# Kernel optimization log

Measured on AMD Instinct MI355X. Metric: run time of the kernel, lower is better.

## Reference

```python
import jax, jax.numpy as jnp
import numpy as np

B, L = 2048, 64          # sentence pairs, leaves per balanced binary tree
V, IN, M, HID, NC = 50000, 300, 150, 50, 5


def setup_inputs() -> dict:
    key = jax.random.key(0)
    ks = jax.random.split(key, 16)
    lin = lambda k, fi, fo: jax.random.normal(k, (fi, fo), jnp.float32) / np.sqrt(fi).astype(np.float32)
    bias = lambda k, fo: jax.random.normal(k, (fo,), jnp.float32) * 0.01
    return {
        "ltokens": jax.random.randint(ks[0], (B, L), 0, V, dtype=jnp.int32),
        "rtokens": jax.random.randint(ks[1], (B, L), 0, V, dtype=jnp.int32),
        "emb":   jax.random.normal(ks[2], (V, IN), jnp.float32),
        "Wioux": lin(ks[3], IN, 3 * M), "bioux": bias(ks[4], 3 * M),
        "Wiouh": lin(ks[5], M, 3 * M), "biouh": bias(ks[6], 3 * M),
        "Wfx":   lin(ks[7], IN, M),    "bfx":   bias(ks[8], M),
        "Wfh":   lin(ks[9], M, M),     "bfh":   bias(ks[10], M),
        "Wh":    lin(ks[11], 2 * M, HID), "bh": bias(ks[12], HID),
        "Wp":    lin(ks[13], HID, NC),    "bp": bias(ks[14], NC),
    }


def _split_iou(iou, m):
    return iou[..., :m], iou[..., m:2 * m], iou[..., 2 * m:]


def _encode(tokens, emb, Wioux, bioux, Wiouh, biouh, Wfh, bfh):
    m = Wfh.shape[0]
    x = emb[tokens]                                   # [B, L, IN]
    # Leaves: child_h = child_c = 0, so iouh contributes only its bias and fc = 0.
    iou = x @ Wioux + bioux + biouh                   # [B, L, 3M]
    i, o, u = _split_iou(iou, m)
    c = jax.nn.sigmoid(i) * jnp.tanh(u)
    h = jax.nn.sigmoid(o) * jnp.tanh(c)
    # Internal nodes level by level (inputs=None branch of node_forward).
    while h.shape[1] > 1:
        Bq, n, _ = h.shape
        ch = h.reshape(Bq, n // 2, 2, m)              # children h
        cc = c.reshape(Bq, n // 2, 2, m)              # children c
        iou = ch.sum(axis=2) @ Wiouh + biouh          # child-sum
        i, o, u = _split_iou(iou, m)
        f = jax.nn.sigmoid(ch @ Wfh + bfh)            # per-child forget gate
        c = jax.nn.sigmoid(i) * jnp.tanh(u) + (f * cc).sum(axis=2)
        h = jax.nn.sigmoid(o) * jnp.tanh(c)
    # ROOT in the original just passes its single child's state through.
    return h[:, 0]                                    # [B, M]


def reference(ltokens, rtokens, emb, Wioux, bioux, Wiouh, biouh, Wfx, bfx, Wfh, bfh, Wh, bh, Wp, bp):
    lh = _encode(ltokens, emb, Wioux, bioux, Wiouh, biouh, Wfh, bfh)
    rh = _encode(rtokens, emb, Wioux, bioux, Wiouh, biouh, Wfh, bfh)
    vec = jnp.concatenate([lh * rh, jnp.abs(lh - rh)], axis=-1)   # [B, 2M]
    mid = jax.nn.sigmoid(vec @ Wh + bh)
    return jax.nn.log_softmax(mid @ Wp + bp, axis=-1)             # [B, NC]
```

## Files before the change

kernel.cpp:

```cpp
#include <hip/hip_runtime.h>
#include <hip/hip_bf16.h>
#include <math.h>

constexpr int B_   = 2048;
constexpr int L_   = 64;
constexpr int V_   = 50000;
constexpr int IN_  = 300;
constexpr int M_   = 150;
constexpr int HID_ = 50;
constexpr int NC_  = 5;

constexpr int KP_  = 160;
constexpr int EN_  = 608;
constexpr int LVL_N  = 608;
constexpr int LVL_NT = 19;
constexpr int LVL_KC = 5;
constexpr int LVL_CH = LVL_N * 32;
constexpr int LVL_QS = LVL_N * 8;
constexpr int LEAF_N  = 480;
constexpr int LEAF_NT = 15;
constexpr int LEAF_KC = 10;
constexpr int LEAF_CH = LEAF_N * 32;
constexpr int LEAF_QS = LEAF_N * 8;

typedef float f32x4  __attribute__((ext_vector_type(4)));
typedef short bf16x8 __attribute__((ext_vector_type(8)));
typedef short short4v __attribute__((ext_vector_type(4)));

__device__ __forceinline__ float rcp_f(float x) { return __builtin_amdgcn_rcpf(x); }
__device__ __forceinline__ float sgm(float x)   { return rcp_f(1.0f + __expf(-x)); }
__device__ __forceinline__ float tanh_f(float x){ return 1.0f - 2.0f * rcp_f(1.0f + __expf(2.0f * x)); }

__device__ __forceinline__ short f2bs(float f) {
    union { __hip_bfloat16 h; short s; } u; u.h = __float2bfloat16(f); return u.s;
}
__device__ __forceinline__ float bs2f(short s) {
    union { short s; __hip_bfloat16 h; } u; u.s = s; return __bfloat162float(u.h);
}

__device__ __forceinline__ void gl_lds16(const short* g, short* l) {
    __builtin_amdgcn_global_load_lds(
        (const __attribute__((address_space(1))) unsigned int*)g,
        (__attribute__((address_space(3))) unsigned int*)l, 16, 0, 0);
}

__global__ __launch_bounds__(256) void prep_kernel(
    const float* __restrict__ Wioux, const float* __restrict__ Wiouh,
    const float* __restrict__ Wfh, short* __restrict__ Bp, short* __restrict__ Bx)
{
    const int tid = blockIdx.x * blockDim.x + threadIdx.x;
    const int nthr = gridDim.x * blockDim.x;
    const int tot1 = LVL_KC * LVL_CH;
    for (int idx = tid; idx < tot1; idx += nthr) {
        const int kc = idx / LVL_CH;
        int rem = idx % LVL_CH;
        const int q = rem / LVL_QS; rem %= LVL_QS;
        const int n = rem / 8, j = rem % 8;
        const int k = kc * 32 + q * 8 + j;
        float v = 0.0f;
        if (k < M_) {
            if (n < 450) v = Wiouh[k * 450 + n];
            else if (n < 600) v = Wfh[k * M_ + (n - 450)];
        }
        Bp[idx] = f2bs(v);
    }
    const int tot2 = LEAF_KC * LEAF_CH;
    for (int idx = tid; idx < tot2; idx += nthr) {
        const int kc = idx / LEAF_CH;
        int rem = idx % LEAF_CH;
        const int q = rem / LEAF_QS; rem %= LEAF_QS;
        const int n = rem / 8, j = rem % 8;
        const int k = kc * 32 + q * 8 + j;
        float v = (k < IN_ && n < 450) ? Wioux[k * 450 + n] : 0.0f;
        Bx[idx] = f2bs(v);
    }
}

__global__ __launch_bounds__(512) void leaf_gemm(
    const float* __restrict__ emb, const short* __restrict__ Bx,
    const float* __restrict__ bioux, const float* __restrict__ biouh,
    short* __restrict__ LeafH, short* __restrict__ LeafC)
{
    __shared__ __align__(16) char smem[LEAF_CH * 2 + 64 * 64];
    short* Bs = (short*)smem;
    short* As = (short*)(smem + LEAF_CH * 2);
    float* Es = (float*)smem;

    const int t = threadIdx.x;
    const int row0 = blockIdx.x * 64;
    const int w = t >> 6, lane = t & 63;
    const int mt = w & 3, nt0 = (w >> 2) * LEAF_NT;
    const int lr = lane & 15, quad = lane >> 4;

    f32x4 acc[LEAF_NT];
    #pragma unroll
    for (int i = 0; i < LEAF_NT; i++) { acc[i][0] = 0; acc[i][1] = 0; acc[i][2] = 0; acc[i][3] = 0; }

    const int arow = t >> 3, apart = t & 7;
    const int av = row0 + arow;
    const int aq = apart >> 1, aj = (apart & 1) * 4;

    for (int kc = 0; kc < LEAF_KC; kc++) {
        const short* bsrc = Bx + (size_t)kc * LEAF_CH;
        #pragma unroll
        for (int i = 0; i < 3; i++)
            gl_lds16(bsrc + (i * 512 + t) * 8, Bs + (i * 512 + (t & ~63)) * 8);
        if (t < 384)
            gl_lds16(bsrc + (1536 + t) * 8, Bs + (1536 + (t & ~63)) * 8);
        {
            const int k0 = kc * 32 + apart * 4;
            float4 x = make_float4(0.f, 0.f, 0.f, 0.f);
            if (av < V_ && k0 < IN_) x = *(const float4*)&emb[(size_t)av * IN_ + k0];
            short4v s;
            s[0] = f2bs(x.x); s[1] = f2bs(x.y); s[2] = f2bs(x.z); s[3] = f2bs(x.w);
            *(short4v*)&As[aq * 512 + arow * 8 + aj] = s;
        }
        __syncthreads();
        bf16x8 a = *(const bf16x8*)&As[quad * 512 + (mt * 16 + lr) * 8];
        #pragma unroll
        for (int i = 0; i < LEAF_NT; i++) {
            bf16x8 b = *(const bf16x8*)&Bs[quad * LEAF_QS + ((nt0 + i) * 16 + lr) * 8];
            acc[i] = __builtin_amdgcn_mfma_f32_16x16x32_bf16(a, b, acc[i], 0, 0, 0);
        }
        __syncthreads();
    }

    for (int mc = 0; mc < 4; mc++) {
        if (mt == mc) {
            #pragma unroll
            for (int i = 0; i < LEAF_NT; i++) {
                const int col = (nt0 + i) * 16 + lr;
                #pragma unroll
                for (int r = 0; r < 4; r++) Es[(quad * 4 + r) * LEAF_N + col] = acc[i][r];
            }
        }
        __syncthreads();
        for (int p = t; p < 16 * KP_; p += 512) {
            const int rl = p / KP_, n = p % KP_;
            const int v = row0 + mc * 16 + rl;
            if (v < V_) {
                if (n < M_) {
                    const float i_ = Es[rl * LEAF_N + n]       + bioux[n]       + biouh[n];
                    const float o_ = Es[rl * LEAF_N + n + 150] + bioux[n + 150] + biouh[n + 150];
                    const float u_ = Es[rl * LEAF_N + n + 300] + bioux[n + 300] + biouh[n + 300];
                    const float c = sgm(i_) * tanh_f(u_);
                    const float h = sgm(o_) * tanh_f(c);
                    LeafH[(size_t)v * KP_ + n] = f2bs(h);
                    LeafC[(size_t)v * KP_ + n] = f2bs(c);
                } else {
                    LeafH[(size_t)v * KP_ + n] = 0;
                    LeafC[(size_t)v * KP_ + n] = 0;
                }
            }
        }
        __syncthreads();
    }
}

__global__ __launch_bounds__(512) void leafGF_gemm(
    const short* __restrict__ LeafH, const short* __restrict__ LeafC,
    const short* __restrict__ Bp, const float* __restrict__ bfh,
    short* __restrict__ LeafE)
{
    __shared__ __align__(16) char smem[LVL_CH * 2 + 64 * 64];
    short* Bs = (short*)smem;
    short* As = (short*)(smem + LVL_CH * 2);
    float* Es = (float*)smem;

    const int t = threadIdx.x;
    const int row0 = blockIdx.x * 64;
    const int w = t >> 6, lane = t & 63;
    const int mt = w & 3, nt0 = (w >> 2) * LVL_NT;
    const int lr = lane & 15, quad = lane >> 4;

    f32x4 acc[LVL_NT];
    #pragma unroll
    for (int i = 0; i < LVL_NT; i++) { acc[i][0] = 0; acc[i][1] = 0; acc[i][2] = 0; acc[i][3] = 0; }

    const int arow = t & 63, apart = t >> 6;
    const size_t srow = (size_t)((row0 + arow < V_) ? (row0 + arow) : 0);
    const short* asrc = LeafH + srow * KP_ + apart * 8;

    for (int kc = 0; kc < LVL_KC; kc++) {
        const short* bsrc = Bp + (size_t)kc * LVL_CH;
        #pragma unroll
        for (int i = 0; i < 4; i++)
            gl_lds16(bsrc + (i * 512 + t) * 8, Bs + (i * 512 + (t & ~63)) * 8);
        if (t < 384)
            gl_lds16(bsrc + (2048 + t) * 8, Bs + (2048 + (t & ~63)) * 8);
        if (t < 256)
            gl_lds16(asrc + kc * 32, As + (t & ~63) * 8);
        __syncthreads();
        bf16x8 a = *(const bf16x8*)&As[quad * 512 + (mt * 16 + lr) * 8];
        #pragma unroll
        for (int i = 0; i < LVL_NT; i++) {
            bf16x8 b = *(const bf16x8*)&Bs[quad * LVL_QS + ((nt0 + i) * 16 + lr) * 8];
            acc[i] = __builtin_amdgcn_mfma_f32_16x16x32_bf16(a, b, acc[i], 0, 0, 0);
        }
        __syncthreads();
    }

    for (int mc = 0; mc < 4; mc++) {
        if (mt == mc) {
            #pragma unroll
            for (int i = 0; i < LVL_NT; i++) {
                const int col = (nt0 + i) * 16 + lr;
                #pragma unroll
                for (int r = 0; r < 4; r++) Es[(quad * 4 + r) * LVL_N + col] = acc[i][r];
            }
        }
        __syncthreads();
        for (int p = t; p < 16 * EN_; p += 512) {
            const int rl = p / EN_, n = p % EN_;
            const int v = row0 + mc * 16 + rl;
            if (v < V_) {
                short outv = 0;
                if (n < 450) {
                    outv = f2bs(Es[rl * LVL_N + n]);
                } else if (n < 600) {
                    const int m = n - 450;
                    const float f = sgm(Es[rl * LVL_N + n] + bfh[m]);
                    outv = f2bs(f * bs2f(LeafC[(size_t)v * KP_ + m]));
                }
                LeafE[(size_t)v * EN_ + n] = outv;
            }
        }
        __syncthreads();
    }
}

__global__ __launch_bounds__(256) void level0_kernel(
    const int* __restrict__ ltok, const int* __restrict__ rtok,
    const short* __restrict__ LeafE, const float* __restrict__ biouh,
    short* __restrict__ Hout, short* __restrict__ Cout)
{
    const int w = threadIdx.x >> 6, lane = threadIdx.x & 63;
    const int nd = blockIdx.x * 4 + w;
    const int g0 = 2 * nd, g1 = g0 + 1;
    const int half = B_ * L_;
    const int tl = (g0 < half) ? ltok[g0] : rtok[g0 - half];
    const int tr = (g1 < half) ? ltok[g1] : rtok[g1 - half];
    const short* el = LeafE + (size_t)tl * EN_;
    const short* er = LeafE + (size_t)tr * EN_;
    for (int m = lane; m < KP_; m += 64) {
        float h = 0.0f, c = 0.0f;
        if (m < M_) {
            const float i_ = bs2f(el[m])       + bs2f(er[m])       + biouh[m];
            const float o_ = bs2f(el[m + 150]) + bs2f(er[m + 150]) + biouh[m + 150];
            const float u_ = bs2f(el[m + 300]) + bs2f(er[m + 300]) + biouh[m + 300];
            const float fc = bs2f(el[m + 450]) + bs2f(er[m + 450]);
            c = sgm(i_) * tanh_f(u_) + fc;
            h = sgm(o_) * tanh_f(c);
        }
        Hout[(size_t)nd * KP_ + m] = f2bs(h);
        Cout[(size_t)nd * KP_ + m] = f2bs(c);
    }
}

__global__ __launch_bounds__(512) void level_gemm(
    const short* __restrict__ Hin, const short* __restrict__ Cin,
    const short* __restrict__ Bp,
    const float* __restrict__ biouh, const float* __restrict__ bfh,
    short* __restrict__ Hout, short* __restrict__ Cout)
{
    __shared__ __align__(16) char smem[LVL_CH * 2 + 64 * 64];
    short* Bs = (short*)smem;
    short* As = (short*)(smem + LVL_CH * 2);
    float* Es = (float*)smem;

    const int t = threadIdx.x;
    const int row0 = blockIdx.x * 64;
    const int w = t >> 6, lane = t & 63;
    const int mt = w & 3, nt0 = (w >> 2) * LVL_NT;
    const int lr = lane & 15, quad = lane >> 4;

    f32x4 acc[LVL_NT];
    #pragma unroll
    for (int i = 0; i < LVL_NT; i++) { acc[i][0] = 0; acc[i][1] = 0; acc[i][2] = 0; acc[i][3] = 0; }

    const int arow = t & 63, apart = t >> 6;
    const short* asrc = Hin + (size_t)(row0 + arow) * KP_ + apart * 8;

    for (int kc = 0; kc < LVL_KC; kc++) {
        const short* bsrc = Bp + (size_t)kc * LVL_CH;
        #pragma unroll
        for (int i = 0; i < 4; i++)
            gl_lds16(bsrc + (i * 512 + t) * 8, Bs + (i * 512 + (t & ~63)) * 8);
        if (t < 384)
            gl_lds16(bsrc + (2048 + t) * 8, Bs + (2048 + (t & ~63)) * 8);
        if (t < 256)
            gl_lds16(asrc + kc * 32, As + (t & ~63) * 8);
        __syncthreads();
        bf16x8 a = *(const bf16x8*)&As[quad * 512 + (mt * 16 + lr) * 8];
        #pragma unroll
        for (int i = 0; i < LVL_NT; i++) {
            bf16x8 b = *(const bf16x8*)&Bs[quad * LVL_QS + ((nt0 + i) * 16 + lr) * 8];
            acc[i] = __builtin_amdgcn_mfma_f32_16x16x32_bf16(a, b, acc[i], 0, 0, 0);
        }
        __syncthreads();
    }

    for (int mc = 0; mc < 4; mc++) {
        if (mt == mc) {
            #pragma unroll
            for (int i = 0; i < LVL_NT; i++) {
                const int col = (nt0 + i) * 16 + lr;
                #pragma unroll
                for (int r = 0; r < 4; r++) Es[(quad * 4 + r) * LVL_N + col] = acc[i][r];
            }
        }
        __syncthreads();
        for (int p = t; p < 8 * KP_; p += 512) {
            const int rl = p / KP_, n = p % KP_;
            const int r_out = blockIdx.x * 32 + mc * 8 + rl;
            if (n < M_) {
                const int e0 = (2 * rl) * LVL_N, e1 = (2 * rl + 1) * LVL_N;
                const float i_ = Es[e0 + n]       + Es[e1 + n]       + biouh[n];
                const float o_ = Es[e0 + n + 150] + Es[e1 + n + 150] + biouh[n + 150];
                const float u_ = Es[e0 + n + 300] + Es[e1 + n + 300] + biouh[n + 300];
                const float fl = Es[e0 + n + 450] + bfh[n];
                const float fr = Es[e1 + n + 450] + bfh[n];
                const int lc0 = mc * 16 + 2 * rl;
                const float cl = bs2f(Cin[(size_t)(row0 + lc0)     * KP_ + n]);
                const float cr = bs2f(Cin[(size_t)(row0 + lc0 + 1) * KP_ + n]);
                const float c = sgm(i_) * tanh_f(u_) + sgm(fl) * cl + sgm(fr) * cr;
                const float h = sgm(o_) * tanh_f(c);
                Hout[(size_t)r_out * KP_ + n] = f2bs(h);
                Cout[(size_t)r_out * KP_ + n] = f2bs(c);
            } else {
                Hout[(size_t)r_out * KP_ + n] = 0;
                Cout[(size_t)r_out * KP_ + n] = 0;
            }
        }
        __syncthreads();
    }
}

__global__ __launch_bounds__(64) void head_kernel(
    const short* __restrict__ RootH,
    const float* __restrict__ Wh, const float* __restrict__ bh,
    const float* __restrict__ Wp, const float* __restrict__ bp,
    float* __restrict__ out)
{
    __shared__ float vec[2 * M_];
    __shared__ float mid[HID_];
    __shared__ float lg[NC_];
    __shared__ float lse;

    const int b = blockIdx.x;
    const int t = threadIdx.x;
    const short* lh = RootH + (size_t)b * KP_;
    const short* rh = RootH + (size_t)(B_ + b) * KP_;

    for (int i = t; i < M_; i += 64) {
        const float a = bs2f(lh[i]), c = bs2f(rh[i]);
        vec[i]      = a * c;
        vec[M_ + i] = fabsf(a - c);
    }
    __syncthreads();

    for (int j = t; j < HID_; j += 64) {
        float acc = bh[j];
        for (int k = 0; k < 2 * M_; k++) acc += vec[k] * Wh[k * HID_ + j];
        mid[j] = sgm(acc);
    }
    __syncthreads();

    if (t < NC_) {
        float acc = bp[t];
        for (int k = 0; k < HID_; k++) acc += mid[k] * Wp[k * NC_ + t];
        lg[t] = acc;
    }
    __syncthreads();

    if (t == 0) {
        float mx = lg[0];
        for (int i = 1; i < NC_; i++) mx = fmaxf(mx, lg[i]);
        float s = 0.0f;
        for (int i = 0; i < NC_; i++) s += expf(lg[i] - mx);
        lse = mx + logf(s);
    }
    __syncthreads();

    if (t < NC_) out[b * NC_ + t] = lg[t] - lse;
}

extern "C" void kernel_launch(void* const* d_in, const int* in_sizes, int n_in,
                              void* d_out, int out_size, void* d_ws, size_t ws_size,
                              hipStream_t stream)
{
    const int*   ltok  = (const int*)d_in[0];
    const int*   rtok  = (const int*)d_in[1];
    const float* emb   = (const float*)d_in[2];
    const float* Wioux = (const float*)d_in[3];
    const float* bioux = (const float*)d_in[4];
    const float* Wiouh = (const float*)d_in[5];
    const float* biouh = (const float*)d_in[6];
    const float* Wfh   = (const float*)d_in[9];
    const float* bfh   = (const float*)d_in[10];
    const float* Wh    = (const float*)d_in[11];
    const float* bh    = (const float*)d_in[12];
    const float* Wp    = (const float*)d_in[13];
    const float* bp    = (const float*)d_in[14];
    float* out = (float*)d_out;

    char* ws = (char*)d_ws;
    size_t off = 0;
    auto carve = [&](size_t bytes) { char* p = ws + off; off += (bytes + 255) & ~(size_t)255; return p; };
    short* Bp    = (short*)carve((size_t)LVL_KC * LVL_CH * 2);
    short* Bx    = (short*)carve((size_t)LEAF_KC * LEAF_CH * 2);
    short* LeafH = (short*)carve((size_t)V_ * KP_ * 2);
    short* LeafC = (short*)carve((size_t)V_ * KP_ * 2);
    short* LeafE = (short*)carve((size_t)V_ * EN_ * 2);
    short* HA    = (short*)carve((size_t)131072 * KP_ * 2);
    short* CA    = (short*)carve((size_t)131072 * KP_ * 2);
    short* HB    = (short*)carve((size_t)65536 * KP_ * 2);
    short* CB    = (short*)carve((size_t)65536 * KP_ * 2);

    hipLaunchKernelGGL(prep_kernel, dim3(128), dim3(256), 0, stream, Wioux, Wiouh, Wfh, Bp, Bx);
    hipLaunchKernelGGL(leaf_gemm, dim3((V_ + 63) / 64), dim3(512), 0, stream,
                       emb, Bx, bioux, biouh, LeafH, LeafC);
    hipLaunchKernelGGL(leafGF_gemm, dim3((V_ + 63) / 64), dim3(512), 0, stream,
                       LeafH, LeafC, Bp, bfh, LeafE);
    hipLaunchKernelGGL(level0_kernel, dim3(32768), dim3(256), 0, stream,
                       ltok, rtok, LeafE, biouh, HA, CA);
    hipLaunchKernelGGL(level_gemm, dim3(2048), dim3(512), 0, stream,
                       HA, CA, Bp, biouh, bfh, HB, CB);
    hipLaunchKernelGGL(level_gemm, dim3(1024), dim3(512), 0, stream,
                       HB, CB, Bp, biouh, bfh, HA, CA);
    hipLaunchKernelGGL(level_gemm, dim3(512), dim3(512), 0, stream,
                       HA, CA, Bp, biouh, bfh, HB, CB);
    hipLaunchKernelGGL(level_gemm, dim3(256), dim3(512), 0, stream,
                       HB, CB, Bp, biouh, bfh, HA, CA);
    hipLaunchKernelGGL(level_gemm, dim3(128), dim3(512), 0, stream,
                       HA, CA, Bp, biouh, bfh, HB, CB);
    hipLaunchKernelGGL(head_kernel, dim3(B_), dim3(64), 0, stream, HB, Wh, bh, Wp, bp, out);
}
```

Before: 575.4 us.

## Fuse level-0 combine into first level GEMM and interleave gate columns for register epilogue

Reorders the packed recurrent weight columns so the i/o/u/f gates of each hidden unit sit adjacent. The level GEMM epilogue can then combine child pairs with wave shuffles in registers instead of staging fp32 results through LDS in four passes. The separate level-0 kernel is folded into a new level-1 kernel that gathers leaf entries by token directly into the LDS A tile, which removes one full-size intermediate H/C round trip through global memory. Child C values are prefetched into LDS, and outputs are written as coalesced 16-byte stores. The cost is more LDS per block and heavier shuffle logic in the epilogue.

```diff
diff --git a/kernel.cpp b/kernel.cpp
--- a/kernel.cpp
+++ b/kernel.cpp
@@ -11,12 +11,11 @@
 constexpr int NC_  = 5;
 
 constexpr int KP_  = 160;
-constexpr int EN_  = 608;
-constexpr int LVL_N  = 608;
-constexpr int LVL_NT = 19;
-constexpr int LVL_KC = 5;
-constexpr int LVL_CH = LVL_N * 32;
-constexpr int LVL_QS = LVL_N * 8;
+constexpr int GN_  = 608;
+constexpr int GNT_ = 19;
+constexpr int GKC_ = 5;
+constexpr int GCH_ = GN_ * 32;
+constexpr int GQS_ = GN_ * 8;
 constexpr int LEAF_N  = 480;
 constexpr int LEAF_NT = 15;
 constexpr int LEAF_KC = 10;
@@ -46,23 +45,22 @@
 
 __global__ __launch_bounds__(256) void prep_kernel(
     const float* __restrict__ Wioux, const float* __restrict__ Wiouh,
-    const float* __restrict__ Wfh, short* __restrict__ Bp, short* __restrict__ Bx)
+    const float* __restrict__ Wfh, short* __restrict__ Bg, short* __restrict__ Bx)
 {
     const int tid = blockIdx.x * blockDim.x + threadIdx.x;
     const int nthr = gridDim.x * blockDim.x;
-    const int tot1 = LVL_KC * LVL_CH;
+    const int tot1 = GKC_ * GCH_;
     for (int idx = tid; idx < tot1; idx += nthr) {
-        const int kc = idx / LVL_CH;
-        int rem = idx % LVL_CH;
-        const int q = rem / LVL_QS; rem %= LVL_QS;
+        const int kc = idx / GCH_;
+        int rem = idx % GCH_;
+        const int q = rem / GQS_; rem %= GQS_;
         const int n = rem / 8, j = rem % 8;
         const int k = kc * 32 + q * 8 + j;
+        const int m = n >> 2, g = n & 3;
         float v = 0.0f;
-        if (k < M_) {
-            if (n < 450) v = Wiouh[k * 450 + n];
-            else if (n < 600) v = Wfh[k * M_ + (n - 450)];
-        }
-        Bp[idx] = f2bs(v);
+        if (k < M_ && m < M_)
+            v = (g < 3) ? Wiouh[k * 450 + g * 150 + m] : Wfh[k * M_ + m];
+        Bg[idx] = f2bs(v);
     }
     const int tot2 = LEAF_KC * LEAF_CH;
     for (int idx = tid; idx < tot2; idx += nthr) {
@@ -159,30 +157,41 @@
 
 __global__ __launch_bounds__(512) void leafGF_gemm(
     const short* __restrict__ LeafH, const short* __restrict__ LeafC,
-    const short* __restrict__ Bp, const float* __restrict__ bfh,
+    const short* __restrict__ Bg, const float* __restrict__ bfh,
     short* __restrict__ LeafE)
 {
-    __shared__ __align__(16) char smem[LVL_CH * 2 + 64 * 64];
-    short* Bs = (short*)smem;
-    short* As = (short*)(smem + LVL_CH * 2);
-    float* Es = (float*)smem;
+    __shared__ __align__(16) char smem[GCH_ * 2 + 4096 + KP_ * 64 * 2 + 600];
+    short* Bs   = (short*)smem;
+    short* As   = (short*)(smem + GCH_ * 2);
+    short* CinS = (short*)(smem + GCH_ * 2 + 4096);
+    float* bfs  = (float*)(smem + GCH_ * 2 + 4096 + KP_ * 64 * 2);
+    short* Os   = Bs;
 
     const int t = threadIdx.x;
-    const int row0 = blockIdx.x * 64;
+    const int v0 = blockIdx.x * 64;
     const int w = t >> 6, lane = t & 63;
-    const int mt = w & 3, nt0 = (w >> 2) * LVL_NT;
+    const int mt = w & 3, nt0 = (w >> 2) * GNT_;
     const int lr = lane & 15, quad = lane >> 4;
-
-    f32x4 acc[LVL_NT];
-    #pragma unroll
-    for (int i = 0; i < LVL_NT; i++) { acc[i][0] = 0; acc[i][1] = 0; acc[i][2] = 0; acc[i][3] = 0; }
+    const int c = lane & 15;
+
+    if (t < 150) bfs[t] = bfh[t];
+    const short* csrc = LeafC + (size_t)v0 * KP_;
+    #pragma unroll
+    for (int i = 0; i < 2; i++)
+        gl_lds16(csrc + (i * 512 + t) * 8, CinS + (i * 512 + (t & ~63)) * 8);
+    if (t < 256)
+        gl_lds16(csrc + (1024 + t) * 8, CinS + (1024 + (t & ~63)) * 8);
+
+    f32x4 acc[GNT_];
+    #pragma unroll
+    for (int i = 0; i < GNT_; i++) { acc[i][0] = 0; acc[i][1] = 0; acc[i][2] = 0; acc[i][3] = 0; }
 
     const int arow = t & 63, apart = t >> 6;
-    const size_t srow = (size_t)((row0 + arow < V_) ? (row0 + arow) : 0);
+    const size_t srow = (size_t)((v0 + arow < V_) ? (v0 + arow) : 0);
     const short* asrc = LeafH + srow * KP_ + apart * 8;
 
-    for (int kc = 0; kc < LVL_KC; kc++) {
-        const short* bsrc = Bp + (size_t)kc * LVL_CH;
+    for (int kc = 0; kc < GKC_; kc++) {
+        const short* bsrc = Bg + (size_t)kc * GCH_;
         #pragma unroll
         for (int i = 0; i < 4; i++)
             gl_lds16(bsrc + (i * 512 + t) * 8, Bs + (i * 512 + (t & ~63)) * 8);
@@ -193,96 +202,210 @@
         __syncthreads();
         bf16x8 a = *(const bf16x8*)&As[quad * 512 + (mt * 16 + lr) * 8];
         #pragma unroll
-        for (int i = 0; i < LVL_NT; i++) {
-            bf16x8 b = *(const bf16x8*)&Bs[quad * LVL_QS + ((nt0 + i) * 16 + lr) * 8];
+        for (int i = 0; i < GNT_; i++) {
+            bf16x8 b = *(const bf16x8*)&Bs[quad * GQS_ + ((nt0 + i) * 16 + lr) * 8];
             acc[i] = __builtin_amdgcn_mfma_f32_16x16x32_bf16(a, b, acc[i], 0, 0, 0);
         }
         __syncthreads();
     }
 
-    for (int mc = 0; mc < 4; mc++) {
-        if (mt == mc) {
+    for (int ph = 0; ph < 2; ph++) {
+        if ((mt >> 1) == ph) {
+            const int rbase = 16 * (mt & 1) + 4 * quad;
             #pragma unroll
-            for (int i = 0; i < LVL_NT; i++) {
-                const int col = (nt0 + i) * 16 + lr;
+            for (int i = 0; i < GNT_; i++) {
+                const int col = (nt0 + i) * 16 + c;
+                const int m = col >> 2, g = col & 3;
                 #pragma unroll
-                for (int r = 0; r < 4; r++) Es[(quad * 4 + r) * LVL_N + col] = acc[i][r];
+                for (int r = 0; r < 4; r++) {
+                    short ov;
+                    if (g == 3) {
+                        if (m < M_) {
+                            const float cc = bs2f(CinS[(32 * ph + rbase + r) * KP_ + m]);
+                            ov = f2bs(sgm(acc[i][r] + bfs[m]) * cc);
+                        } else ov = 0;
+                    } else ov = f2bs(acc[i][r]);
+                    Os[(rbase + r) * GN_ + col] = ov;
+                }
             }
         }
         __syncthreads();
-        for (int p = t; p < 16 * EN_; p += 512) {
-            const int rl = p / EN_, n = p % EN_;
-            const int v = row0 + mc * 16 + rl;
-            if (v < V_) {
-                short outv = 0;
-                if (n < 450) {
-                    outv = f2bs(Es[rl * LVL_N + n]);
-                } else if (n < 600) {
-                    const int m = n - 450;
-                    const float f = sgm(Es[rl * LVL_N + n] + bfh[m]);
-                    outv = f2bs(f * bs2f(LeafC[(size_t)v * KP_ + m]));
+        const int vb = v0 + 32 * ph;
+        const int4* os4 = (const int4*)Os;
+        for (int u = t; u < 2432; u += 512) {
+            const int row = u / 76;
+            if (vb + row < V_)
+                ((int4*)(LeafE + (size_t)(vb + row) * GN_))[u - row * 76] = os4[u];
+        }
+        __syncthreads();
+    }
+}
+
+__device__ __forceinline__ void level_epilogue(
+    const f32x4* acc, int mt, int nt0, int lane,
+    const short* CinS, const float* bias_s, short* Hs, short* Cs)
+{
+    const int q = lane >> 4, c = lane & 15, g = c & 3, lb = lane & ~3;
+    #pragma unroll
+    for (int i = 0; i < GNT_; i++) {
+        const int col = (nt0 + i) * 16 + c;
+        const int m = col >> 2;
+        const float vA = acc[i][0] + acc[i][1];
+        const float vB = acc[i][2] + acc[i][3];
+        const float iA = __shfl(vA, lb), oA = __shfl(vA, lb + 1), uA = __shfl(vA, lb + 2);
+        const float iB = __shfl(vB, lb), oB = __shfl(vB, lb + 1), uB = __shfl(vB, lb + 2);
+        const float fA0 = __shfl(acc[i][0], lb + 3), fA1 = __shfl(acc[i][1], lb + 3);
+        const float fB0 = __shfl(acc[i][2], lb + 3), fB1 = __shfl(acc[i][3], lb + 3);
+        if (g < 2 && m < M_) {
+            const float iv = g ? iB : iA, ov = g ? oB : oA, uv = g ? uB : uA;
+            const float fl = g ? fB0 : fA0, fr = g ? fB1 : fA1;
+            const int node = 8 * mt + 2 * q + g;
+            const int ch = 16 * mt + 4 * q + 2 * g;
+            const float cl = bs2f(CinS[ch * KP_ + m]);
+            const float cr = bs2f(CinS[(ch + 1) * KP_ + m]);
+            const float bf = bias_s[450 + m];
+            const float cv = sgm(iv + bias_s[m]) * tanh_f(uv + bias_s[m + 300])
+                           + sgm(fl + bf) * cl + sgm(fr + bf) * cr;
+            const float hv = sgm(ov + bias_s[m + 150]) * tanh_f(cv);
+            Hs[node * KP_ + m] = f2bs(hv);
+            Cs[node * KP_ + m] = f2bs(cv);
+        }
+    }
+}
+
+__global__ __launch_bounds__(512) void level1_fused(
+    const int* __restrict__ ltok, const int* __restrict__ rtok,
+    const short* __restrict__ LeafE, const short* __restrict__ Bg,
+    const float* __restrict__ biouh, const float* __restrict__ bfh,
+    short* __restrict__ Hout, short* __restrict__ Cout)
+{
+    __shared__ __align__(16) char smem[GCH_ * 2 + 20480 + 20480 + 2400 + 512];
+    short* Bs     = (short*)smem;
+    short* AsF    = (short*)(smem + GCH_ * 2);
+    short* CinS   = (short*)(smem + GCH_ * 2 + 20480);
+    float* bias_s = (float*)(smem + GCH_ * 2 + 40960);
+    int*   toks   = (int*)(smem + GCH_ * 2 + 43360);
+    short* Hs = Bs;
+    short* Cs = Bs + 32 * KP_;
+
+    const int t = threadIdx.x;
+    const int out0 = blockIdx.x * 32;
+    const int w = t >> 6, lane = t & 63;
+    const int mt = w & 3, nt0 = (w >> 2) * GNT_;
+    const int lr = lane & 15, quad = lane >> 4;
+
+    if (t < 600) bias_s[t] = (t < 450) ? biouh[t] : bfh[t - 450];
+    if (t < 128) {
+        const int idx = blockIdx.x * 128 + t;
+        toks[t] = (idx < B_ * L_) ? ltok[idx] : rtok[idx - B_ * L_];
+    }
+    __syncthreads();
+
+    {
+        const int row = t >> 3, qs = t & 7;
+        const short* el = LeafE + (size_t)toks[2 * row] * GN_;
+        const short* er = LeafE + (size_t)toks[2 * row + 1] * GN_;
+        #pragma unroll
+        for (int s = 0; s < 5; s++) {
+            const int Q = qs + 8 * s;
+            short4v hq = {0, 0, 0, 0}, cq = {0, 0, 0, 0};
+            if (Q < 38) {
+                union { int4 v[2]; short s16[16]; } ue, ur;
+                ue.v[0] = *(const int4*)(el + Q * 16);
+                ue.v[1] = *(const int4*)(el + Q * 16 + 8);
+                ur.v[0] = *(const int4*)(er + Q * 16);
+                ur.v[1] = *(const int4*)(er + Q * 16 + 8);
+                #pragma unroll
+                for (int jj = 0; jj < 4; jj++) {
+                    const int m = 4 * Q + jj;
+                    if (m < M_) {
+                        const float i_ = bs2f(ue.s16[4 * jj])     + bs2f(ur.s16[4 * jj])     + bias_s[m];
+                        const float o_ = bs2f(ue.s16[4 * jj + 1]) + bs2f(ur.s16[4 * jj + 1]) + bias_s[m + 150];
+                        const float u_ = bs2f(ue.s16[4 * jj + 2]) + bs2f(ur.s16[4 * jj + 2]) + bias_s[m + 300];
+                        const float fc = bs2f(ue.s16[4 * jj + 3]) + bs2f(ur.s16[4 * jj + 3]);
+                        const float cv = sgm(i_) * tanh_f(u_) + fc;
+                        const float hv = sgm(o_) * tanh_f(cv);
+                        hq[jj] = f2bs(hv); cq[jj] = f2bs(cv);
+                    }
                 }
-                LeafE[(size_t)v * EN_ + n] = outv;
             }
-        }
-        __syncthreads();
-    }
-}
-
-__global__ __launch_bounds__(256) void level0_kernel(
-    const int* __restrict__ ltok, const int* __restrict__ rtok,
-    const short* __restrict__ LeafE, const float* __restrict__ biouh,
-    short* __restrict__ Hout, short* __restrict__ Cout)
-{
-    const int w = threadIdx.x >> 6, lane = threadIdx.x & 63;
-    const int nd = blockIdx.x * 4 + w;
-    const int g0 = 2 * nd, g1 = g0 + 1;
-    const int half = B_ * L_;
-    const int tl = (g0 < half) ? ltok[g0] : rtok[g0 - half];
-    const int tr = (g1 < half) ? ltok[g1] : rtok[g1 - half];
-    const short* el = LeafE + (size_t)tl * EN_;
-    const short* er = LeafE + (size_t)tr * EN_;
-    for (int m = lane; m < KP_; m += 64) {
-        float h = 0.0f, c = 0.0f;
-        if (m < M_) {
-            const float i_ = bs2f(el[m])       + bs2f(er[m])       + biouh[m];
-            const float o_ = bs2f(el[m + 150]) + bs2f(er[m + 150]) + biouh[m + 150];
-            const float u_ = bs2f(el[m + 300]) + bs2f(er[m + 300]) + biouh[m + 300];
-            const float fc = bs2f(el[m + 450]) + bs2f(er[m + 450]);
-            c = sgm(i_) * tanh_f(u_) + fc;
-            h = sgm(o_) * tanh_f(c);
-        }
-        Hout[(size_t)nd * KP_ + m] = f2bs(h);
-        Cout[(size_t)nd * KP_ + m] = f2bs(c);
+            const int m0 = 4 * Q;
+            const int kc = m0 >> 5, q = (m0 >> 3) & 3, j0 = m0 & 7;
+            *(short4v*)&AsF[(kc * 4 + q) * 512 + row * 8 + j0] = hq;
+            *(short4v*)&CinS[row * KP_ + m0] = cq;
+        }
+    }
+
+    f32x4 acc[GNT_];
+    #pragma unroll
+    for (int i = 0; i < GNT_; i++) { acc[i][0] = 0; acc[i][1] = 0; acc[i][2] = 0; acc[i][3] = 0; }
+
+    for (int kc = 0; kc < GKC_; kc++) {
+        const short* bsrc = Bg + (size_t)kc * GCH_;
+        #pragma unroll
+        for (int i = 0; i < 4; i++)
+            gl_lds16(bsrc + (i * 512 + t) * 8, Bs + (i * 512 + (t & ~63)) * 8);
+        if (t < 384)
+            gl_lds16(bsrc + (2048 + t) * 8, Bs + (2048 + (t & ~63)) * 8);
+        __syncthreads();
+        bf16x8 a = *(const bf16x8*)&AsF[kc * 2048 + quad * 512 + (mt * 16 + lr) * 8];
+        #pragma unroll
+        for (int i = 0; i < GNT_; i++) {
+            bf16x8 b = *(const bf16x8*)&Bs[quad * GQS_ + ((nt0 + i) * 16 + lr) * 8];
+            acc[i] = __builtin_amdgcn_mfma_f32_16x16x32_bf16(a, b, acc[i], 0, 0, 0);
+        }
+        __syncthreads();
+    }
+
+    if (t < 320) { const int node = t / 10, mm = 150 + t % 10;
+                   Hs[node * KP_ + mm] = 0; Cs[node * KP_ + mm] = 0; }
+    level_epilogue(acc, mt, nt0, lane, CinS, bias_s, Hs, Cs);
+    __syncthreads();
+    int4* Hg = (int4*)(Hout + (size_t)out0 * KP_);
+    int4* Cg = (int4*)(Cout + (size_t)out0 * KP_);
+    const int4* hs4 = (const int4*)Hs;
+    const int4* cs4 = (const int4*)Cs;
+    for (int u = t; u < 1280; u += 512) {
+        if (u < 640) Hg[u] = hs4[u]; else Cg[u - 640] = cs4[u - 640];
     }
 }
 
 __global__ __launch_bounds__(512) void level_gemm(
     const short* __restrict__ Hin, const short* __restrict__ Cin,
-    const short* __restrict__ Bp,
+    const short* __restrict__ Bg,
     const float* __restrict__ biouh, const float* __restrict__ bfh,
     short* __restrict__ Hout, short* __restrict__ Cout)
 {
-    __shared__ __align__(16) char smem[LVL_CH * 2 + 64 * 64];
-    short* Bs = (short*)smem;
-    short* As = (short*)(smem + LVL_CH * 2);
-    float* Es = (float*)smem;
+    __shared__ __align__(16) char smem[GCH_ * 2 + 4096 + 20480 + 2400];
+    short* Bs     = (short*)smem;
+    short* As     = (short*)(smem + GCH_ * 2);
+    short* CinS   = (short*)(smem + GCH_ * 2 + 4096);
+    float* bias_s = (float*)(smem + GCH_ * 2 + 4096 + 20480);
+    short* Hs = Bs;
+    short* Cs = Bs + 32 * KP_;
 
     const int t = threadIdx.x;
-    const int row0 = blockIdx.x * 64;
+    const int row0 = blockIdx.x * 64, out0 = blockIdx.x * 32;
     const int w = t >> 6, lane = t & 63;
-    const int mt = w & 3, nt0 = (w >> 2) * LVL_NT;
+    const int mt = w & 3, nt0 = (w >> 2) * GNT_;
     const int lr = lane & 15, quad = lane >> 4;
 
-    f32x4 acc[LVL_NT];
-    #pragma unroll
-    for (int i = 0; i < LVL_NT; i++) { acc[i][0] = 0; acc[i][1] = 0; acc[i][2] = 0; acc[i][3] = 0; }
-
-    const int arow = t & 63, apart = t >> 6;
-    const short* asrc = Hin + (size_t)(row0 + arow) * KP_ + apart * 8;
-
-    for (int kc = 0; kc < LVL_KC; kc++) {
-        const short* bsrc = Bp + (size_t)kc * LVL_CH;
+    if (t < 600) bias_s[t] = (t < 450) ? biouh[t] : bfh[t - 450];
+    const short* csrc = Cin + (size_t)row0 * KP_;
+    #pragma unroll
+    for (int i = 0; i < 2; i++)
+        gl_lds16(csrc + (i * 512 + t) * 8, CinS + (i * 512 + (t & ~63)) * 8);
+    if (t < 256)
+        gl_lds16(csrc + (1024 + t) * 8, CinS + (1024 + (t & ~63)) * 8);
+
+    f32x4 acc[GNT_];
+    #pragma unroll
+    for (int i = 0; i < GNT_; i++) { acc[i][0] = 0; acc[i][1] = 0; acc[i][2] = 0; acc[i][3] = 0; }
+
+    const short* asrc = Hin + (size_t)(row0 + (t & 63)) * KP_ + (t >> 6) * 8;
+
+    for (int kc = 0; kc < GKC_; kc++) {
+        const short* bsrc = Bg + (size_t)kc * GCH_;
         #pragma unroll
         for (int i = 0; i < 4; i++)
             gl_lds16(bsrc + (i * 512 + t) * 8, Bs + (i * 512 + (t & ~63)) * 8);
@@ -293,46 +416,23 @@
         __syncthreads();
         bf16x8 a = *(const bf16x8*)&As[quad * 512 + (mt * 16 + lr) * 8];
         #pragma unroll
-        for (int i = 0; i < LVL_NT; i++) {
-            bf16x8 b = *(const bf16x8*)&Bs[quad * LVL_QS + ((nt0 + i) * 16 + lr) * 8];
+        for (int i = 0; i < GNT_; i++) {
+            bf16x8 b = *(const bf16x8*)&Bs[quad * GQS_ + ((nt0 + i) * 16 + lr) * 8];
             acc[i] = __builtin_amdgcn_mfma_f32_16x16x32_bf16(a, b, acc[i], 0, 0, 0);
         }
         __syncthreads();
     }
 
-    for (int mc = 0; mc < 4; mc++) {
-        if (mt == mc) {
-            #pragma unroll
-            for (int i = 0; i < LVL_NT; i++) {
-                const int col = (nt0 + i) * 16 + lr;
-                #pragma unroll
-                for (int r = 0; r < 4; r++) Es[(quad * 4 + r) * LVL_N + col] = acc[i][r];
-            }
-        }
-        __syncthreads();
-        for (int p = t; p < 8 * KP_; p += 512) {
-            const int rl = p / KP_, n = p % KP_;
-            const int r_out = blockIdx.x * 32 + mc * 8 + rl;
-            if (n < M_) {
-                const int e0 = (2 * rl) * LVL_N, e1 = (2 * rl + 1) * LVL_N;
-                const float i_ = Es[e0 + n]       + Es[e1 + n]       + biouh[n];
-                const float o_ = Es[e0 + n + 150] + Es[e1 + n + 150] + biouh[n + 150];
-                const float u_ = Es[e0 + n + 300] + Es[e1 + n + 300] + biouh[n + 300];
-                const float fl = Es[e0 + n + 450] + bfh[n];
-                const float fr = Es[e1 + n + 450] + bfh[n];
-                const int lc0 = mc * 16 + 2 * rl;
-                const float cl = bs2f(Cin[(size_t)(row0 + lc0)     * KP_ + n]);
-                const float cr = bs2f(Cin[(size_t)(row0 + lc0 + 1) * KP_ + n]);
-                const float c = sgm(i_) * tanh_f(u_) + sgm(fl) * cl + sgm(fr) * cr;
-                const float h = sgm(o_) * tanh_f(c);
-                Hout[(size_t)r_out * KP_ + n] = f2bs(h);
-                Cout[(size_t)r_out * KP_ + n] = f2bs(c);
-            } else {
-                Hout[(size_t)r_out * KP_ + n] = 0;
-                Cout[(size_t)r_out * KP_ + n] = 0;
-            }
-        }
-        __syncthreads();
+    if (t < 320) { const int node = t / 10, mm = 150 + t % 10;
+                   Hs[node * KP_ + mm] = 0; Cs[node * KP_ + mm] = 0; }
+    level_epilogue(acc, mt, nt0, lane, CinS, bias_s, Hs, Cs);
+    __syncthreads();
+    int4* Hg = (int4*)(Hout + (size_t)out0 * KP_);
+    int4* Cg = (int4*)(Cout + (size_t)out0 * KP_);
+    const int4* hs4 = (const int4*)Hs;
+    const int4* cs4 = (const int4*)Cs;
+    for (int u = t; u < 1280; u += 512) {
+        if (u < 640) Hg[u] = hs4[u]; else Cg[u - 640] = cs4[u - 640];
     }
 }
 
@@ -407,32 +507,30 @@
     char* ws = (char*)d_ws;
     size_t off = 0;
     auto carve = [&](size_t bytes) { char* p = ws + off; off += (bytes + 255) & ~(size_t)255; return p; };
-    short* Bp    = (short*)carve((size_t)LVL_KC * LVL_CH * 2);
+    short* Bg    = (short*)carve((size_t)GKC_ * GCH_ * 2);
     short* Bx    = (short*)carve((size_t)LEAF_KC * LEAF_CH * 2);
     short* LeafH = (short*)carve((size_t)V_ * KP_ * 2);
     short* LeafC = (short*)carve((size_t)V_ * KP_ * 2);
-    short* LeafE = (short*)carve((size_t)V_ * EN_ * 2);
-    short* HA    = (short*)carve((size_t)131072 * KP_ * 2);
-    short* CA    = (short*)carve((size_t)131072 * KP_ * 2);
-    short* HB    = (short*)carve((size_t)65536 * KP_ * 2);
-    short* CB    = (short*)carve((size_t)65536 * KP_ * 2);
-
-    hipLaunchKernelGGL(prep_kernel, dim3(128), dim3(256), 0, stream, Wioux, Wiouh, Wfh, Bp, Bx);
+    short* LeafE = (short*)carve((size_t)V_ * GN_ * 2);
+    short* HA    = (short*)carve((size_t)65536 * KP_ * 2);
+    short* CA    = (short*)carve((size_t)65536 * KP_ * 2);
+    short* HB    = (short*)carve((size_t)32768 * KP_ * 2);
+    short* CB    = (short*)carve((size_t)32768 * KP_ * 2);
+
+    hipLaunchKernelGGL(prep_kernel, dim3(128), dim3(256), 0, stream, Wioux, Wiouh, Wfh, Bg, Bx);
     hipLaunchKernelGGL(leaf_gemm, dim3((V_ + 63) / 64), dim3(512), 0, stream,
                        emb, Bx, bioux, biouh, LeafH, LeafC);
     hipLaunchKernelGGL(leafGF_gemm, dim3((V_ + 63) / 64), dim3(512), 0, stream,
-                       LeafH, LeafC, Bp, bfh, LeafE);
-    hipLaunchKernelGGL(level0_kernel, dim3(32768), dim3(256), 0, stream,
-                       ltok, rtok, LeafE, biouh, HA, CA);
-    hipLaunchKernelGGL(level_gemm, dim3(2048), dim3(512), 0, stream,
-                       HA, CA, Bp, biouh, bfh, HB, CB);
+                       LeafH, LeafC, Bg, bfh, LeafE);
+    hipLaunchKernelGGL(level1_fused, dim3(2048), dim3(512), 0, stream,
+                       ltok, rtok, LeafE, Bg, biouh, bfh, HA, CA);
     hipLaunchKernelGGL(level_gemm, dim3(1024), dim3(512), 0, stream,
-                       HB, CB, Bp, biouh, bfh, HA, CA);
+                       HA, CA, Bg, biouh, bfh, HB, CB);
     hipLaunchKernelGGL(level_gemm, dim3(512), dim3(512), 0, stream,
-                       HA, CA, Bp, biouh, bfh, HB, CB);
+                       HB, CB, Bg, biouh, bfh, HA, CA);
     hipLaunchKernelGGL(level_gemm, dim3(256), dim3(512), 0, stream,
-                       HB, CB, Bp, biouh, bfh, HA, CA);
+                       HA, CA, Bg, biouh, bfh, HB, CB);
     hipLaunchKernelGGL(level_gemm, dim3(128), dim3(512), 0, stream,
-                       HA, CA, Bp, biouh, bfh, HB, CB);
-    hipLaunchKernelGGL(head_kernel, dim3(B_), dim3(64), 0, stream, HB, Wh, bh, Wp, bp, out);
-}
+                       HB, CB, Bg, biouh, bfh, HA, CA);
+    hipLaunchKernelGGL(head_kernel, dim3(B_), dim3(64), 0, stream, HA, Wh, bh, Wp, bp, out);
+}
```

New measurement: 537.2 us. -6.6%, faster.
